# Optimization experiments

Hardware: AMD Instinct MI355X
Metric: run time of the kernel (lower is better)

## Reference

```python
import jax, jax.numpy as jnp
import numpy as np
from jax import lax

B, C, H, W, T = 8, 512, 96, 96, 4
EPS = 1e-5


def setup_inputs() -> dict:
    key = jax.random.key(0)
    k1, k2, k3 = jax.random.split(key, 3)
    x = jax.random.normal(k1, (B, C, H, W), dtype=jnp.float32)
    # grouped 1x1 conv, groups=2: torch weight [C, C//2, 1, 1] -> [2, C//2(out), C//2(in)]
    w_mix = jax.random.normal(k2, (2, C // 2, C // 2), dtype=jnp.float32) * (1.0 / np.sqrt(C // 2))
    # depthwise 3x3: torch weight [C, 1, 3, 3]
    w_dw = jax.random.normal(k3, (C, 1, 3, 3), dtype=jnp.float32) * (1.0 / 3.0)
    gammas = jnp.ones((T, 1, C, 1, 1), dtype=jnp.float32)
    betas = jnp.zeros((T, 1, C, 1, 1), dtype=jnp.float32)
    alpha = jnp.float32(0.25)
    return {"x": x, "w_mix": w_mix, "w_dw": w_dw, "gammas": gammas, "betas": betas, "alpha": alpha}


def _entropy_gate(x):
    gate = jnp.zeros_like(x)
    for d in (1, 2, 4):
        gate = gate + jnp.abs(x - jnp.roll(x, d, axis=2)) + jnp.abs(x - jnp.roll(x, d, axis=3))
    return jax.nn.sigmoid(gate / 3.0)


def reference(x, w_mix, w_dw, gammas, betas, alpha):
    b, c, h_, w_ = x.shape
    x_prev = x
    for t in range(T):
        gate = _entropy_gate(x)
        # grouped 1x1 conv (groups=2): [B,2,C/2,H,W] x [2,Co,Ci] -> [B,2,Co,H,W]
        xg = x.reshape(b, 2, c // 2, h_, w_)
        h = jnp.einsum('bgihw,goi->bgohw', xg, w_mix)
        # channel shuffle: view(B,2,C/2,H,W).transpose(1,2).reshape(B,C,H,W)
        h = h.transpose(0, 2, 1, 3, 4).reshape(b, c, h_, w_)
        # depthwise 3x3, padding=1
        h = lax.conv_general_dilated(h, w_dw, window_strides=(1, 1), padding=((1, 1), (1, 1)),
                                     feature_group_count=c,
                                     dimension_numbers=('NCHW', 'OIHW', 'NCHW'))
        # instance norm (no affine, eps=1e-5) then per-step affine
        mu = jnp.mean(h, axis=(2, 3), keepdims=True)
        var = jnp.mean(jnp.square(h - mu), axis=(2, 3), keepdims=True)
        h = (h - mu) * lax.rsqrt(var + EPS) * gammas[t] + betas[t]
        h = jax.nn.gelu(h, approximate=False)
        x_new = x + gate * h + alpha * (x - x_prev)
        x_prev = x
        x = x_new
    return x
```

## Files before the change

kernel.cpp:

```cpp
#include <hip/hip_runtime.h>
#include <hip/hip_bf16.h>
#include <cstddef>

#define IMW   96
#define HWSZ  (IMW*IMW)
#define CTOT  512
#define CHG   256
#define NBATCH 8
#define ROWP  104
#define XT_LD 280
#define TO_LD 76

typedef short  bf16x8  __attribute__((ext_vector_type(8)));
typedef float  f32x4   __attribute__((ext_vector_type(4)));
typedef unsigned short ushort8v __attribute__((ext_vector_type(8)));
typedef _Float16 f16x2 __attribute__((ext_vector_type(2)));
typedef __fp16   fp16x2b __attribute__((ext_vector_type(2)));

union U32H2 { unsigned u; f16x2 h; fp16x2b hb; };

__device__ __forceinline__ unsigned pk2(float lo, float hi) {
    union { __hip_bfloat162 h; unsigned u; } v;
    v.h = __float22bfloat162_rn(make_float2(lo, hi));
    return v.u;
}
__device__ __forceinline__ unsigned pkh(float lo, float hi) {
    U32H2 v; v.hb = __builtin_amdgcn_cvt_pkrtz(lo, hi); return v.u;
}
__device__ __forceinline__ f16x2 h2(unsigned u) { U32H2 v; v.u = u; return v.h; }
__device__ __forceinline__ unsigned h2u(f16x2 h) { U32H2 v; v.h = h; return v.u; }
__device__ __forceinline__ float bf2f(ushort u) {
    union { unsigned u; float f; } v; v.u = ((unsigned)u) << 16;
    return v.f;
}

__global__ __launch_bounds__(256) void wconv_kernel(const float* __restrict__ w,
                                                    unsigned* __restrict__ wbf) {
    const int i = blockIdx.x * 256 + threadIdx.x;
    wbf[i] = pk2(w[2 * i], w[2 * i + 1]);
}

template<bool XB>
__global__ __launch_bounds__(256, 3) void mix_mfma(
    const void* __restrict__ xin, const ushort* __restrict__ wbf,
    ushort* __restrict__ h)
{
    const int pt = blockIdx.x * 64;
    const int b  = blockIdx.y >> 1, g = blockIdx.y & 1;
    const size_t xoff = ((size_t)b * CTOT + (size_t)g * CHG) * HWSZ;
    const ushort* wg = wbf + (size_t)g * CHG * CHG;
    ushort* hb = h + (size_t)b * CTOT * HWSZ;

    __shared__ ushort XtBuf[19456];

    const int t  = threadIdx.x;
    const int tq = t & 15;
    const int tk = t >> 4;

    #pragma unroll
    for (int it = 0; it < 8; ++it) {
        const int k = 32 * it + 2 * tk;
        unsigned u0, u1, u2, u3;
        if constexpr (XB) {
            const ushort* xb = (const ushort*)xin + xoff;
            ushort4 a0 = *(const ushort4*)&xb[(size_t)k       * HWSZ + pt + 4 * tq];
            ushort4 a1 = *(const ushort4*)&xb[(size_t)(k + 1) * HWSZ + pt + 4 * tq];
            u0 = (unsigned)a0.x | ((unsigned)a1.x << 16);
            u1 = (unsigned)a0.y | ((unsigned)a1.y << 16);
            u2 = (unsigned)a0.z | ((unsigned)a1.z << 16);
            u3 = (unsigned)a0.w | ((unsigned)a1.w << 16);
        } else {
            const float* xb = (const float*)xin + xoff;
            float4 a0 = *(const float4*)&xb[(size_t)k       * HWSZ + pt + 4 * tq];
            float4 a1 = *(const float4*)&xb[(size_t)(k + 1) * HWSZ + pt + 4 * tq];
            u0 = pk2(a0.x, a1.x);
            u1 = pk2(a0.y, a1.y);
            u2 = pk2(a0.z, a1.z);
            u3 = pk2(a0.w, a1.w);
        }
        *(unsigned*)&XtBuf[(4 * tq + 0) * XT_LD + k] = u0;
        *(unsigned*)&XtBuf[(4 * tq + 1) * XT_LD + k] = u1;
        *(unsigned*)&XtBuf[(4 * tq + 2) * XT_LD + k] = u2;
        *(unsigned*)&XtBuf[(4 * tq + 3) * XT_LD + k] = u3;
    }
    __syncthreads();

    const int wv  = t >> 6;
    const int ln  = t & 63;
    const int row = ln & 15;
    const int kb  = ln >> 4;

    f32x4 acc[4][4];
    #pragma unroll
    for (int m = 0; m < 4; ++m)
        #pragma unroll
        for (int n = 0; n < 4; ++n)
            acc[m][n] = (f32x4){0.f, 0.f, 0.f, 0.f};

    #pragma unroll
    for (int ks = 0; ks < 8; ++ks) {
        bf16x8 Xf[4], Wf[4];
        #pragma unroll
        for (int m = 0; m < 4; ++m)
            Xf[m] = *(const bf16x8*)&XtBuf[(16 * m + row) * XT_LD + 32 * ks + 8 * kb];
        #pragma unroll
        for (int n = 0; n < 4; ++n)
            Wf[n] = *(const bf16x8*)&wg[(size_t)(64 * wv + 16 * n + row) * CHG + 32 * ks + 8 * kb];
        #pragma unroll
        for (int m = 0; m < 4; ++m)
            #pragma unroll
            for (int n = 0; n < 4; ++n)
                acc[m][n] = __builtin_amdgcn_mfma_f32_16x16x32_bf16(Xf[m], Wf[n], acc[m][n], 0, 0, 0);
    }

    __syncthreads();
    #pragma unroll
    for (int m = 0; m < 4; ++m) {
        #pragma unroll
        for (int n = 0; n < 4; ++n) {
            const int o = 64 * wv + 16 * n + row;
            *(uint2*)&XtBuf[o * TO_LD + 16 * m + 4 * kb] =
                make_uint2(pkh(acc[m][n][0], acc[m][n][1]), pkh(acc[m][n][2], acc[m][n][3]));
        }
    }
    __syncthreads();
    const int o8i = t >> 3;
    const int px8 = (t & 7) * 8;
    #pragma unroll
    for (int j = 0; j < 8; ++j) {
        const int o2 = o8i + 32 * j;
        const int c  = 2 * o2 + g;
        uint4 v = *(const uint4*)&XtBuf[o2 * TO_LD + px8];
        *(uint4*)&hb[(size_t)c * HWSZ + pt + px8] = v;
    }
}

template<bool XB, bool PB, bool EQ, bool OB>
__global__ __launch_bounds__(576, 4) void plane_kernel(
    const ushort* __restrict__ hmid,
    const void* __restrict__ xcur, const void* __restrict__ xprev,
    const float* __restrict__ wdw,
    const float* __restrict__ gammas, const float* __restrict__ betas,
    const float* __restrict__ alphap, int t,
    void* __restrict__ out)
{
    const int plane = blockIdx.x;
    const int c = plane & (CTOT - 1);
    const ushort* hp = hmid + (size_t)plane * HWSZ;

    __shared__ ushort sh[IMW * ROWP];
    __shared__ ushort sx[IMW * ROWP];
    __shared__ float  red[32];

    const int tid = threadIdx.x;
    const int r   = tid / 6;
    const int s6  = tid - r * 6;
    const int x0  = s6 * 16;
    const int pix = r * IMW + x0;

    ushort8v xr[2];
    float4   xf[4];
    float xv[16];
    if constexpr (XB) {
        const ushort8v* s = (const ushort8v*)((const ushort*)xcur + (size_t)plane * HWSZ + pix);
        xr[0] = s[0]; xr[1] = s[1];
        #pragma unroll
        for (int j = 0; j < 8; ++j) { xv[j] = bf2f(xr[0][j]); xv[8 + j] = bf2f(xr[1][j]); }
    } else {
        const float4* s = (const float4*)((const float*)xcur + (size_t)plane * HWSZ + pix);
        #pragma unroll
        for (int q = 0; q < 4; ++q) xf[q] = s[q];
        #pragma unroll
        for (int q = 0; q < 4; ++q)
            #pragma unroll
            for (int j = 0; j < 4; ++j) xv[4 * q + j] = xf[q][j];
    }
    {
        const uint4* src = (const uint4*)(hp + (size_t)r * IMW);
        uint4* dst = (uint4*)(sh + r * ROWP);
        dst[2 * s6]     = src[2 * s6];
        dst[2 * s6 + 1] = src[2 * s6 + 1];
    }
    {
        uint4* dst = (uint4*)(sx + r * ROWP + x0);
        dst[0] = make_uint4(pkh(xv[0], xv[1]),  pkh(xv[2], xv[3]),
                            pkh(xv[4], xv[5]),  pkh(xv[6], xv[7]));
        dst[1] = make_uint4(pkh(xv[8], xv[9]),  pkh(xv[10], xv[11]),
                            pkh(xv[12], xv[13]), pkh(xv[14], xv[15]));
    }
    float w9[9];
    #pragma unroll
    for (int i = 0; i < 9; ++i) w9[i] = wdw[c * 9 + i];

    __syncthreads();

    ushort8v pr[2];
    float4   pf[4];
    if constexpr (!EQ) {
        if constexpr (PB) {
            const ushort8v* s = (const ushort8v*)((const ushort*)xprev + (size_t)plane * HWSZ + pix);
            pr[0] = s[0]; pr[1] = s[1];
        } else {
            const float4* s = (const float4*)((const float*)xprev + (size_t)plane * HWSZ + pix);
            #pragma unroll
            for (int q = 0; q < 4; ++q) pf[q] = s[q];
        }
    }

    f16x2 cp[8];
    #pragma unroll
    for (int m = 0; m < 8; ++m) cp[m] = (f16x2){(_Float16)0.f, (_Float16)0.f};
    #pragma unroll
    for (int ky = 0; ky < 3; ++ky) {
        const int yy = r + ky - 1;
        if ((unsigned)yy < IMW) {
            const ushort* rp = sh + yy * ROWP + x0;
            uint4 ga = *(const uint4*)rp;
            uint4 gb = *(const uint4*)(rp + 8);
            unsigned gg[8] = {ga.x, ga.y, ga.z, ga.w, gb.x, gb.y, gb.z, gb.w};
            const unsigned L = (s6 > 0) ? *(const unsigned*)(rp - 2)  : 0u;
            const unsigned R = (s6 < 5) ? *(const unsigned*)(rp + 16) : 0u;
            unsigned S[9];
            S[0] = (L >> 16) | (gg[0] << 16);
            #pragma unroll
            for (int m = 1; m < 8; ++m) S[m] = (gg[m - 1] >> 16) | (gg[m] << 16);
            S[8] = (gg[7] >> 16) | (R << 16);
            const _Float16 w0 = (_Float16)w9[3 * ky], w1 = (_Float16)w9[3 * ky + 1],
                           w2 = (_Float16)w9[3 * ky + 2];
            const f16x2 w0_2 = (f16x2){w0, w0}, w1_2 = (f16x2){w1, w1}, w2_2 = (f16x2){w2, w2};
            #pragma unroll
            for (int m = 0; m < 8; ++m)
                cp[m] = cp[m] + w0_2 * h2(S[m]) + w1_2 * h2(gg[m]) + w2_2 * h2(S[m + 1]);
        }
    }
    float conv[16];
    #pragma unroll
    for (int m = 0; m < 8; ++m) { conv[2 * m] = (float)cp[m][0]; conv[2 * m + 1] = (float)cp[m][1]; }

    f16x2 gt2[8];
    #pragma unroll
    for (int m = 0; m < 8; ++m) gt2[m] = (f16x2){(_Float16)0.f, (_Float16)0.f};
    {
        const ushort* xrp = sx + r * ROWP + x0;
        uint4 xa = *(const uint4*)xrp;
        uint4 xb2 = *(const uint4*)(xrp + 8);
        unsigned xc[8] = {xa.x, xa.y, xa.z, xa.w, xb2.x, xb2.y, xb2.z, xb2.w};
        const int lx1 = (x0 == 0) ? (IMW - 2) : (x0 - 2);
        const int lx2 = (x0 == 0) ? (IMW - 4) : (x0 - 4);
        const unsigned L1 = *(const unsigned*)(sx + r * ROWP + lx1);
        const unsigned L2 = *(const unsigned*)(sx + r * ROWP + lx2);
        unsigned p1[8], p2[8], p4[8];
        p1[0] = (L1 >> 16) | (xc[0] << 16);
        #pragma unroll
        for (int m = 1; m < 8; ++m) p1[m] = (xc[m - 1] >> 16) | (xc[m] << 16);
        p2[0] = L1;
        #pragma unroll
        for (int m = 1; m < 8; ++m) p2[m] = xc[m - 1];
        p4[0] = L2; p4[1] = L1;
        #pragma unroll
        for (int m = 2; m < 8; ++m) p4[m] = xc[m - 2];
        #pragma unroll
        for (int m = 0; m < 8; ++m) {
            const f16x2 xcm = h2(xc[m]);
            gt2[m] = gt2[m] + h2(h2u(xcm - h2(p1[m])) & 0x7FFF7FFFu);
            gt2[m] = gt2[m] + h2(h2u(xcm - h2(p2[m])) & 0x7FFF7FFFu);
            gt2[m] = gt2[m] + h2(h2u(xcm - h2(p4[m])) & 0x7FFF7FFFu);
        }
        #pragma unroll
        for (int dd = 0; dd < 3; ++dd) {
            int ym = r - (1 << dd); if (ym < 0) ym += IMW;
            const ushort* vp = sx + ym * ROWP + x0;
            uint4 va = *(const uint4*)vp;
            uint4 vb = *(const uint4*)(vp + 8);
            unsigned vv[8] = {va.x, va.y, va.z, va.w, vb.x, vb.y, vb.z, vb.w};
            #pragma unroll
            for (int m = 0; m < 8; ++m)
                gt2[m] = gt2[m] + h2(h2u(h2(xc[m]) - h2(vv[m])) & 0x7FFF7FFFu);
        }
    }
    float gt[16];
    #pragma unroll
    for (int m = 0; m < 8; ++m) { gt[2 * m] = (float)gt2[m][0]; gt[2 * m + 1] = (float)gt2[m][1]; }

    float s = 0.f, s2 = 0.f;
    #pragma unroll
    for (int i = 0; i < 16; ++i) { s += conv[i]; s2 = fmaf(conv[i], conv[i], s2); }
    #pragma unroll
    for (int off = 32; off; off >>= 1) {
        s  += __shfl_down(s, off, 64);
        s2 += __shfl_down(s2, off, 64);
    }
    const int wv = tid >> 6;
    if ((tid & 63) == 0) { red[wv] = s; red[16 + wv] = s2; }
    __syncthreads();
    float ssum = 0.f, s2sum = 0.f;
    #pragma unroll
    for (int i = 0; i < 9; ++i) { ssum += red[i]; s2sum += red[16 + i]; }
    const float mu   = ssum * (1.f / HWSZ);
    const float var  = fmaxf(s2sum * (1.f / HWSZ) - mu * mu, 0.f);
    const float rsig = rsqrtf(var + 1e-5f);
    const float ga = gammas[t * CTOT + c] * rsig;
    const float be = betas[t * CTOT + c];
    const float alpha = alphap[0];

    #pragma unroll
    for (int half = 0; half < 2; ++half) {
        float pvh[8];
        if constexpr (EQ) {
            #pragma unroll
            for (int j = 0; j < 8; ++j) pvh[j] = xv[8 * half + j];
        } else if constexpr (PB) {
            #pragma unroll
            for (int j = 0; j < 8; ++j) pvh[j] = bf2f(pr[half][j]);
        } else {
            #pragma unroll
            for (int j = 0; j < 4; ++j) { pvh[j] = pf[2 * half][j]; pvh[4 + j] = pf[2 * half + 1][j]; }
        }
        float o8[8];
        #pragma unroll
        for (int i = 0; i < 8; ++i) {
            const int ii = 8 * half + i;
            const float xvi = xv[ii];
            const float hn  = fmaf(conv[ii] - mu, ga, be);
            const float z2  = 1.5957691216f * fmaf(0.044715f * hn * hn, hn, hn);
            const float ea  = __expf(gt[ii] * (-1.f / 3.f));
            const float eb  = __expf(-z2);
            const float den = (1.f + ea) * (1.f + eb);
            const float gg  = hn * __builtin_amdgcn_rcpf(den);
            o8[i] = fmaf(alpha, xvi - pvh[i], xvi + gg);
        }
        if constexpr (OB) {
            uint4 u = make_uint4(pk2(o8[0], o8[1]), pk2(o8[2], o8[3]),
                                 pk2(o8[4], o8[5]), pk2(o8[6], o8[7]));
            *(uint4*)((ushort*)out + (size_t)plane * HWSZ + pix + 8 * half) = u;
        } else {
            float* op = (float*)out + (size_t)plane * HWSZ + pix + 8 * half;
            *(float4*)op       = make_float4(o8[0], o8[1], o8[2], o8[3]);
            *(float4*)(op + 4) = make_float4(o8[4], o8[5], o8[6], o8[7]);
        }
    }
}

extern "C" void kernel_launch(void* const* d_in, const int* in_sizes, int n_in,
                              void* d_out, int out_size, void* d_ws, size_t ws_size,
                              hipStream_t stream) {
    const float* x0     = (const float*)d_in[0];
    const float* wmix   = (const float*)d_in[1];
    const float* wdw    = (const float*)d_in[2];
    const float* gammas = (const float*)d_in[3];
    const float* betas  = (const float*)d_in[4];
    const float* alphap = (const float*)d_in[5];

    const size_t NELEM = (size_t)NBATCH * CTOT * HWSZ;
    float*  D   = (float*)d_out;
    char*   ws  = (char*)d_ws;
    ushort* X1b = (ushort*)ws;
    ushort* X2b = (ushort*)(ws + NELEM * 2);
    ushort* Hb  = (ushort*)(ws + NELEM * 4);
    ushort* Wbf = (ushort*)(ws + NELEM * 6);

    wconv_kernel<<<256, 256, 0, stream>>>(wmix, (unsigned*)Wbf);

    dim3 mgrid(HWSZ / 64, NBATCH * 2);
    const int pgrid = NBATCH * CTOT;

    mix_mfma<false><<<mgrid, 256, 0, stream>>>(x0, Wbf, Hb);
    plane_kernel<false, false, true, true><<<pgrid, 576, 0, stream>>>(
        Hb, x0, x0, wdw, gammas, betas, alphap, 0, X1b);
    mix_mfma<true><<<mgrid, 256, 0, stream>>>(X1b, Wbf, Hb);
    plane_kernel<true, false, false, true><<<pgrid, 576, 0, stream>>>(
        Hb, X1b, x0, wdw, gammas, betas, alphap, 1, X2b);
    mix_mfma<true><<<mgrid, 256, 0, stream>>>(X2b, Wbf, Hb);
    plane_kernel<true, true, false, true><<<pgrid, 576, 0, stream>>>(
        Hb, X2b, X1b, wdw, gammas, betas, alphap, 2, X1b);
    mix_mfma<true><<<mgrid, 256, 0, stream>>>(X1b, Wbf, Hb);
    plane_kernel<true, true, false, false><<<pgrid, 576, 0, stream>>>(
        Hb, X1b, X2b, wdw, gammas, betas, alphap, 3, D);
}
```

Baseline: 556.2 us.

## Switch intermediates to fp16, process two planes per block, stash x0 in output buffer

Replaces bf16 storage and MFMA with fp16 (mfma 16x16x32 f16) for weights, activations and intermediate states. The depthwise plane kernel now handles two batch planes per block, prefetching the second plane's h and x while the first is computed, and splits the exp of the gate into an fp16-packed precompute. x0 is converted to fp16 once and stashed in the output buffer so later steps read half-precision x_prev instead of fp32. This cuts memory traffic and hides latency, at the cost of fp16 range/precision risk and more register pressure.

```diff
diff --git a/kernel.cpp b/kernel.cpp
--- a/kernel.cpp
+++ b/kernel.cpp
@@ -11,44 +11,34 @@
 #define XT_LD 280
 #define TO_LD 76
 
-typedef short  bf16x8  __attribute__((ext_vector_type(8)));
-typedef float  f32x4   __attribute__((ext_vector_type(4)));
-typedef unsigned short ushort8v __attribute__((ext_vector_type(8)));
-typedef _Float16 f16x2 __attribute__((ext_vector_type(2)));
+typedef float    f32x4  __attribute__((ext_vector_type(4)));
+typedef _Float16 f16x8  __attribute__((ext_vector_type(8)));
+typedef _Float16 f16x2  __attribute__((ext_vector_type(2)));
 typedef __fp16   fp16x2b __attribute__((ext_vector_type(2)));
 
 union U32H2 { unsigned u; f16x2 h; fp16x2b hb; };
 
-__device__ __forceinline__ unsigned pk2(float lo, float hi) {
-    union { __hip_bfloat162 h; unsigned u; } v;
-    v.h = __float22bfloat162_rn(make_float2(lo, hi));
-    return v.u;
-}
 __device__ __forceinline__ unsigned pkh(float lo, float hi) {
     U32H2 v; v.hb = __builtin_amdgcn_cvt_pkrtz(lo, hi); return v.u;
 }
 __device__ __forceinline__ f16x2 h2(unsigned u) { U32H2 v; v.u = u; return v.h; }
 __device__ __forceinline__ unsigned h2u(f16x2 h) { U32H2 v; v.h = h; return v.u; }
-__device__ __forceinline__ float bf2f(ushort u) {
-    union { unsigned u; float f; } v; v.u = ((unsigned)u) << 16;
-    return v.f;
-}
 
 __global__ __launch_bounds__(256) void wconv_kernel(const float* __restrict__ w,
-                                                    unsigned* __restrict__ wbf) {
+                                                    unsigned* __restrict__ wh) {
     const int i = blockIdx.x * 256 + threadIdx.x;
-    wbf[i] = pk2(w[2 * i], w[2 * i + 1]);
+    wh[i] = pkh(w[2 * i], w[2 * i + 1]);
 }
 
 template<bool XB>
 __global__ __launch_bounds__(256, 3) void mix_mfma(
-    const void* __restrict__ xin, const ushort* __restrict__ wbf,
+    const void* __restrict__ xin, const ushort* __restrict__ wh,
     ushort* __restrict__ h)
 {
     const int pt = blockIdx.x * 64;
     const int b  = blockIdx.y >> 1, g = blockIdx.y & 1;
     const size_t xoff = ((size_t)b * CTOT + (size_t)g * CHG) * HWSZ;
-    const ushort* wg = wbf + (size_t)g * CHG * CHG;
+    const ushort* wg = wh + (size_t)g * CHG * CHG;
     ushort* hb = h + (size_t)b * CTOT * HWSZ;
 
     __shared__ ushort XtBuf[19456];
@@ -73,10 +63,10 @@
             const float* xb = (const float*)xin + xoff;
             float4 a0 = *(const float4*)&xb[(size_t)k       * HWSZ + pt + 4 * tq];
             float4 a1 = *(const float4*)&xb[(size_t)(k + 1) * HWSZ + pt + 4 * tq];
-            u0 = pk2(a0.x, a1.x);
-            u1 = pk2(a0.y, a1.y);
-            u2 = pk2(a0.z, a1.z);
-            u3 = pk2(a0.w, a1.w);
+            u0 = pkh(a0.x, a1.x);
+            u1 = pkh(a0.y, a1.y);
+            u2 = pkh(a0.z, a1.z);
+            u3 = pkh(a0.w, a1.w);
         }
         *(unsigned*)&XtBuf[(4 * tq + 0) * XT_LD + k] = u0;
         *(unsigned*)&XtBuf[(4 * tq + 1) * XT_LD + k] = u1;
@@ -99,18 +89,18 @@
 
     #pragma unroll
     for (int ks = 0; ks < 8; ++ks) {
-        bf16x8 Xf[4], Wf[4];
+        f16x8 Xf[4], Wf[4];
         #pragma unroll
         for (int m = 0; m < 4; ++m)
-            Xf[m] = *(const bf16x8*)&XtBuf[(16 * m + row) * XT_LD + 32 * ks + 8 * kb];
+            Xf[m] = *(const f16x8*)&XtBuf[(16 * m + row) * XT_LD + 32 * ks + 8 * kb];
         #pragma unroll
         for (int n = 0; n < 4; ++n)
-            Wf[n] = *(const bf16x8*)&wg[(size_t)(64 * wv + 16 * n + row) * CHG + 32 * ks + 8 * kb];
+            Wf[n] = *(const f16x8*)&wg[(size_t)(64 * wv + 16 * n + row) * CHG + 32 * ks + 8 * kb];
         #pragma unroll
         for (int m = 0; m < 4; ++m)
             #pragma unroll
             for (int n = 0; n < 4; ++n)
-                acc[m][n] = __builtin_amdgcn_mfma_f32_16x16x32_bf16(Xf[m], Wf[n], acc[m][n], 0, 0, 0);
+                acc[m][n] = __builtin_amdgcn_mfma_f32_16x16x32_f16(Xf[m], Wf[n], acc[m][n], 0, 0, 0);
     }
 
     __syncthreads();
@@ -135,79 +125,11 @@
     }
 }
 
-template<bool XB, bool PB, bool EQ, bool OB>
-__global__ __launch_bounds__(576, 4) void plane_kernel(
-    const ushort* __restrict__ hmid,
-    const void* __restrict__ xcur, const void* __restrict__ xprev,
-    const float* __restrict__ wdw,
-    const float* __restrict__ gammas, const float* __restrict__ betas,
-    const float* __restrict__ alphap, int t,
-    void* __restrict__ out)
+__device__ __forceinline__ void plane_partA(
+    const ushort* __restrict__ sh, const ushort* __restrict__ sx,
+    float* __restrict__ red, int tid, int r, int s6, int x0,
+    const float* __restrict__ wc, f16x2 (&cp)[8], unsigned (&ea)[8])
 {
-    const int plane = blockIdx.x;
-    const int c = plane & (CTOT - 1);
-    const ushort* hp = hmid + (size_t)plane * HWSZ;
-
-    __shared__ ushort sh[IMW * ROWP];
-    __shared__ ushort sx[IMW * ROWP];
-    __shared__ float  red[32];
-
-    const int tid = threadIdx.x;
-    const int r   = tid / 6;
-    const int s6  = tid - r * 6;
-    const int x0  = s6 * 16;
-    const int pix = r * IMW + x0;
-
-    ushort8v xr[2];
-    float4   xf[4];
-    float xv[16];
-    if constexpr (XB) {
-        const ushort8v* s = (const ushort8v*)((const ushort*)xcur + (size_t)plane * HWSZ + pix);
-        xr[0] = s[0]; xr[1] = s[1];
-        #pragma unroll
-        for (int j = 0; j < 8; ++j) { xv[j] = bf2f(xr[0][j]); xv[8 + j] = bf2f(xr[1][j]); }
-    } else {
-        const float4* s = (const float4*)((const float*)xcur + (size_t)plane * HWSZ + pix);
-        #pragma unroll
-        for (int q = 0; q < 4; ++q) xf[q] = s[q];
-        #pragma unroll
-        for (int q = 0; q < 4; ++q)
-            #pragma unroll
-            for (int j = 0; j < 4; ++j) xv[4 * q + j] = xf[q][j];
-    }
-    {
-        const uint4* src = (const uint4*)(hp + (size_t)r * IMW);
-        uint4* dst = (uint4*)(sh + r * ROWP);
-        dst[2 * s6]     = src[2 * s6];
-        dst[2 * s6 + 1] = src[2 * s6 + 1];
-    }
-    {
-        uint4* dst = (uint4*)(sx + r * ROWP + x0);
-        dst[0] = make_uint4(pkh(xv[0], xv[1]),  pkh(xv[2], xv[3]),
-                            pkh(xv[4], xv[5]),  pkh(xv[6], xv[7]));
-        dst[1] = make_uint4(pkh(xv[8], xv[9]),  pkh(xv[10], xv[11]),
-                            pkh(xv[12], xv[13]), pkh(xv[14], xv[15]));
-    }
-    float w9[9];
-    #pragma unroll
-    for (int i = 0; i < 9; ++i) w9[i] = wdw[c * 9 + i];
-
-    __syncthreads();
-
-    ushort8v pr[2];
-    float4   pf[4];
-    if constexpr (!EQ) {
-        if constexpr (PB) {
-            const ushort8v* s = (const ushort8v*)((const ushort*)xprev + (size_t)plane * HWSZ + pix);
-            pr[0] = s[0]; pr[1] = s[1];
-        } else {
-            const float4* s = (const float4*)((const float*)xprev + (size_t)plane * HWSZ + pix);
-            #pragma unroll
-            for (int q = 0; q < 4; ++q) pf[q] = s[q];
-        }
-    }
-
-    f16x2 cp[8];
     #pragma unroll
     for (int m = 0; m < 8; ++m) cp[m] = (f16x2){(_Float16)0.f, (_Float16)0.f};
     #pragma unroll
@@ -215,9 +137,9 @@
         const int yy = r + ky - 1;
         if ((unsigned)yy < IMW) {
             const ushort* rp = sh + yy * ROWP + x0;
-            uint4 ga = *(const uint4*)rp;
-            uint4 gb = *(const uint4*)(rp + 8);
-            unsigned gg[8] = {ga.x, ga.y, ga.z, ga.w, gb.x, gb.y, gb.z, gb.w};
+            uint4 ga4 = *(const uint4*)rp;
+            uint4 gb4 = *(const uint4*)(rp + 8);
+            unsigned gg[8] = {ga4.x, ga4.y, ga4.z, ga4.w, gb4.x, gb4.y, gb4.z, gb4.w};
             const unsigned L = (s6 > 0) ? *(const unsigned*)(rp - 2)  : 0u;
             const unsigned R = (s6 < 5) ? *(const unsigned*)(rp + 16) : 0u;
             unsigned S[9];
@@ -225,26 +147,22 @@
             #pragma unroll
             for (int m = 1; m < 8; ++m) S[m] = (gg[m - 1] >> 16) | (gg[m] << 16);
             S[8] = (gg[7] >> 16) | (R << 16);
-            const _Float16 w0 = (_Float16)w9[3 * ky], w1 = (_Float16)w9[3 * ky + 1],
-                           w2 = (_Float16)w9[3 * ky + 2];
+            const _Float16 w0 = (_Float16)wc[3 * ky], w1 = (_Float16)wc[3 * ky + 1],
+                           w2 = (_Float16)wc[3 * ky + 2];
             const f16x2 w0_2 = (f16x2){w0, w0}, w1_2 = (f16x2){w1, w1}, w2_2 = (f16x2){w2, w2};
             #pragma unroll
             for (int m = 0; m < 8; ++m)
                 cp[m] = cp[m] + w0_2 * h2(S[m]) + w1_2 * h2(gg[m]) + w2_2 * h2(S[m + 1]);
         }
     }
-    float conv[16];
-    #pragma unroll
-    for (int m = 0; m < 8; ++m) { conv[2 * m] = (float)cp[m][0]; conv[2 * m + 1] = (float)cp[m][1]; }
-
     f16x2 gt2[8];
     #pragma unroll
     for (int m = 0; m < 8; ++m) gt2[m] = (f16x2){(_Float16)0.f, (_Float16)0.f};
     {
         const ushort* xrp = sx + r * ROWP + x0;
-        uint4 xa = *(const uint4*)xrp;
-        uint4 xb2 = *(const uint4*)(xrp + 8);
-        unsigned xc[8] = {xa.x, xa.y, xa.z, xa.w, xb2.x, xb2.y, xb2.z, xb2.w};
+        uint4 xa4 = *(const uint4*)xrp;
+        uint4 xb4 = *(const uint4*)(xrp + 8);
+        unsigned xc[8] = {xa4.x, xa4.y, xa4.z, xa4.w, xb4.x, xb4.y, xb4.z, xb4.w};
         const int lx1 = (x0 == 0) ? (IMW - 2) : (x0 - 2);
         const int lx2 = (x0 == 0) ? (IMW - 4) : (x0 - 4);
         const unsigned L1 = *(const unsigned*)(sx + r * ROWP + lx1);
@@ -278,67 +196,194 @@
                 gt2[m] = gt2[m] + h2(h2u(h2(xc[m]) - h2(vv[m])) & 0x7FFF7FFFu);
         }
     }
-    float gt[16];
-    #pragma unroll
-    for (int m = 0; m < 8; ++m) { gt[2 * m] = (float)gt2[m][0]; gt[2 * m + 1] = (float)gt2[m][1]; }
-
+    #pragma unroll
+    for (int m = 0; m < 8; ++m)
+        ea[m] = pkh(__expf((float)gt2[m][0] * (-1.f / 3.f)),
+                    __expf((float)gt2[m][1] * (-1.f / 3.f)));
     float s = 0.f, s2 = 0.f;
     #pragma unroll
-    for (int i = 0; i < 16; ++i) { s += conv[i]; s2 = fmaf(conv[i], conv[i], s2); }
+    for (int m = 0; m < 8; ++m) {
+        const float c0 = (float)cp[m][0], c1 = (float)cp[m][1];
+        s += c0 + c1;
+        s2 = fmaf(c0, c0, fmaf(c1, c1, s2));
+    }
     #pragma unroll
     for (int off = 32; off; off >>= 1) {
         s  += __shfl_down(s, off, 64);
         s2 += __shfl_down(s2, off, 64);
     }
-    const int wv = tid >> 6;
-    if ((tid & 63) == 0) { red[wv] = s; red[16 + wv] = s2; }
-    __syncthreads();
-    float ssum = 0.f, s2sum = 0.f;
-    #pragma unroll
-    for (int i = 0; i < 9; ++i) { ssum += red[i]; s2sum += red[16 + i]; }
-    const float mu   = ssum * (1.f / HWSZ);
-    const float var  = fmaxf(s2sum * (1.f / HWSZ) - mu * mu, 0.f);
-    const float rsig = rsqrtf(var + 1e-5f);
-    const float ga = gammas[t * CTOT + c] * rsig;
-    const float be = betas[t * CTOT + c];
+    if ((tid & 63) == 0) { red[tid >> 6] = s; red[16 + (tid >> 6)] = s2; }
+}
+
+template<bool EQv, bool OF32v, bool WRXv>
+__device__ __forceinline__ void plane_tail(
+    const ushort* __restrict__ sx, int r, int x0,
+    const f16x2 (&cp)[8], const unsigned (&ea)[8],
+    uint4 pva, uint4 pvb,
+    float mu, float ga, float be, float alpha,
+    size_t gidx, void* __restrict__ out, ushort* __restrict__ xaux)
+{
+    const ushort* xrp = sx + r * ROWP + x0;
+    const uint4 xqa = *(const uint4*)xrp;
+    const uint4 xqb = *(const uint4*)(xrp + 8);
+    const unsigned xu[8] = {xqa.x, xqa.y, xqa.z, xqa.w, xqb.x, xqb.y, xqb.z, xqb.w};
+    unsigned pu[8];
+    if constexpr (!EQv) {
+        pu[0] = pva.x; pu[1] = pva.y; pu[2] = pva.z; pu[3] = pva.w;
+        pu[4] = pvb.x; pu[5] = pvb.y; pu[6] = pvb.z; pu[7] = pvb.w;
+    }
+    float o[16];
+    #pragma unroll
+    for (int m = 0; m < 8; ++m) {
+        const f16x2 xh = h2(xu[m]);
+        const float xv0 = (float)xh[0], xv1 = (float)xh[1];
+        const float c0 = (float)cp[m][0], c1 = (float)cp[m][1];
+        const f16x2 eh = h2(ea[m]);
+        const float e0 = (float)eh[0], e1 = (float)eh[1];
+        const float hn0 = fmaf(c0 - mu, ga, be);
+        const float hn1 = fmaf(c1 - mu, ga, be);
+        const float z20 = 1.5957691216f * fmaf(0.044715f * hn0 * hn0, hn0, hn0);
+        const float z21 = 1.5957691216f * fmaf(0.044715f * hn1 * hn1, hn1, hn1);
+        const float eb0 = __expf(-z20), eb1 = __expf(-z21);
+        const float gg0 = hn0 * __builtin_amdgcn_rcpf((1.f + e0) * (1.f + eb0));
+        const float gg1 = hn1 * __builtin_amdgcn_rcpf((1.f + e1) * (1.f + eb1));
+        float pv0, pv1;
+        if constexpr (EQv) { pv0 = xv0; pv1 = xv1; }
+        else { const f16x2 ph = h2(pu[m]); pv0 = (float)ph[0]; pv1 = (float)ph[1]; }
+        o[2 * m]     = fmaf(alpha, xv0 - pv0, xv0 + gg0);
+        o[2 * m + 1] = fmaf(alpha, xv1 - pv1, xv1 + gg1);
+    }
+    if constexpr (OF32v) {
+        float* op = (float*)out + gidx;
+        *(float4*)(op)      = make_float4(o[0],  o[1],  o[2],  o[3]);
+        *(float4*)(op + 4)  = make_float4(o[4],  o[5],  o[6],  o[7]);
+        *(float4*)(op + 8)  = make_float4(o[8],  o[9],  o[10], o[11]);
+        *(float4*)(op + 12) = make_float4(o[12], o[13], o[14], o[15]);
+    } else {
+        ushort* op = (ushort*)out + gidx;
+        *(uint4*)op       = make_uint4(pkh(o[0], o[1]),   pkh(o[2], o[3]),
+                                       pkh(o[4], o[5]),   pkh(o[6], o[7]));
+        *(uint4*)(op + 8) = make_uint4(pkh(o[8], o[9]),   pkh(o[10], o[11]),
+                                       pkh(o[12], o[13]), pkh(o[14], o[15]));
+    }
+    if constexpr (WRXv) {
+        ushort* xp = xaux + gidx;
+        *(uint4*)xp = xqa; *(uint4*)(xp + 8) = xqb;
+    }
+}
+
+template<bool XF32, bool EQ, bool OF32, bool WRX>
+__global__ __launch_bounds__(576, 4) void plane2_kernel(
+    const ushort* __restrict__ hmid,
+    const void* __restrict__ xcur, const ushort* __restrict__ xprev,
+    const float* __restrict__ wdw,
+    const float* __restrict__ gammas, const float* __restrict__ betas,
+    const float* __restrict__ alphap, int t,
+    void* __restrict__ out, ushort* __restrict__ xaux)
+{
+    __shared__ ushort sh[IMW * ROWP];
+    __shared__ ushort sx[IMW * ROWP];
+    __shared__ float  red[32];
+
+    const int tid = threadIdx.x;
+    const int r   = tid / 6;
+    const int s6  = tid - r * 6;
+    const int x0  = s6 * 16;
+    const int pix = r * IMW + x0;
+    const int c   = blockIdx.x & (CTOT - 1);
+    const int bp  = blockIdx.x >> 9;
+    const size_t off0 = ((size_t)(2 * bp) * CTOT + c) * HWSZ;
+    const size_t off1 = off0 + (size_t)CTOT * HWSZ;
+
+    const float gam   = gammas[t * CTOT + c];
+    const float be    = betas[t * CTOT + c];
     const float alpha = alphap[0];
-
-    #pragma unroll
-    for (int half = 0; half < 2; ++half) {
-        float pvh[8];
-        if constexpr (EQ) {
+    const float* wc   = wdw + c * 9;
+
+    {
+        uint4 xa0, xb0;
+        if constexpr (XF32) {
+            const float4* s = (const float4*)((const float*)xcur + off0 + pix);
+            float4 v0 = s[0], v1 = s[1], v2 = s[2], v3 = s[3];
+            xa0 = make_uint4(pkh(v0.x, v0.y), pkh(v0.z, v0.w), pkh(v1.x, v1.y), pkh(v1.z, v1.w));
+            xb0 = make_uint4(pkh(v2.x, v2.y), pkh(v2.z, v2.w), pkh(v3.x, v3.y), pkh(v3.z, v3.w));
+        } else {
+            const uint4* s = (const uint4*)((const ushort*)xcur + off0 + pix);
+            xa0 = s[0]; xb0 = s[1];
+        }
+        const uint4* hs = (const uint4*)(hmid + off0 + (size_t)r * IMW);
+        uint4 h00 = hs[2 * s6], h01 = hs[2 * s6 + 1];
+        uint4* hd = (uint4*)(sh + r * ROWP);
+        hd[2 * s6] = h00; hd[2 * s6 + 1] = h01;
+        uint4* xd = (uint4*)(sx + r * ROWP + x0);
+        xd[0] = xa0; xd[1] = xb0;
+    }
+    uint4 h10, h11, xa1, xb1;
+    float4 xf1[4];
+    {
+        const uint4* hs = (const uint4*)(hmid + off1 + (size_t)r * IMW);
+        h10 = hs[2 * s6]; h11 = hs[2 * s6 + 1];
+        if constexpr (XF32) {
+            const float4* s = (const float4*)((const float*)xcur + off1 + pix);
             #pragma unroll
-            for (int j = 0; j < 8; ++j) pvh[j] = xv[8 * half + j];
-        } else if constexpr (PB) {
-            #pragma unroll
-            for (int j = 0; j < 8; ++j) pvh[j] = bf2f(pr[half][j]);
+            for (int q = 0; q < 4; ++q) xf1[q] = s[q];
         } else {
-            #pragma unroll
-            for (int j = 0; j < 4; ++j) { pvh[j] = pf[2 * half][j]; pvh[4 + j] = pf[2 * half + 1][j]; }
-        }
-        float o8[8];
-        #pragma unroll
-        for (int i = 0; i < 8; ++i) {
-            const int ii = 8 * half + i;
-            const float xvi = xv[ii];
-            const float hn  = fmaf(conv[ii] - mu, ga, be);
-            const float z2  = 1.5957691216f * fmaf(0.044715f * hn * hn, hn, hn);
-            const float ea  = __expf(gt[ii] * (-1.f / 3.f));
-            const float eb  = __expf(-z2);
-            const float den = (1.f + ea) * (1.f + eb);
-            const float gg  = hn * __builtin_amdgcn_rcpf(den);
-            o8[i] = fmaf(alpha, xvi - pvh[i], xvi + gg);
-        }
-        if constexpr (OB) {
-            uint4 u = make_uint4(pk2(o8[0], o8[1]), pk2(o8[2], o8[3]),
-                                 pk2(o8[4], o8[5]), pk2(o8[6], o8[7]));
-            *(uint4*)((ushort*)out + (size_t)plane * HWSZ + pix + 8 * half) = u;
-        } else {
-            float* op = (float*)out + (size_t)plane * HWSZ + pix + 8 * half;
-            *(float4*)op       = make_float4(o8[0], o8[1], o8[2], o8[3]);
-            *(float4*)(op + 4) = make_float4(o8[4], o8[5], o8[6], o8[7]);
-        }
-    }
+            const uint4* s = (const uint4*)((const ushort*)xcur + off1 + pix);
+            xa1 = s[0]; xb1 = s[1];
+        }
+    }
+    __syncthreads();
+
+    uint4 pa0, pb0;
+    if constexpr (!EQ) {
+        const uint4* s = (const uint4*)(xprev + off0 + pix);
+        pa0 = s[0]; pb0 = s[1];
+    }
+    f16x2 cp[8]; unsigned ea[8];
+    plane_partA(sh, sx, red, tid, r, s6, x0, wc, cp, ea);
+    __syncthreads();
+    float mu, ga;
+    {
+        float ssum = 0.f, s2sum = 0.f;
+        #pragma unroll
+        for (int q = 0; q < 9; ++q) { ssum += red[q]; s2sum += red[16 + q]; }
+        mu = ssum * (1.f / HWSZ);
+        const float var = fmaxf(s2sum * (1.f / HWSZ) - mu * mu, 0.f);
+        ga = gam * rsqrtf(var + 1e-5f);
+    }
+    plane_tail<EQ, OF32, WRX>(sx, r, x0, cp, ea, pa0, pb0, mu, ga, be, alpha,
+                              off0 + pix, out, xaux);
+    if constexpr (XF32) {
+        xa1 = make_uint4(pkh(xf1[0].x, xf1[0].y), pkh(xf1[0].z, xf1[0].w),
+                         pkh(xf1[1].x, xf1[1].y), pkh(xf1[1].z, xf1[1].w));
+        xb1 = make_uint4(pkh(xf1[2].x, xf1[2].y), pkh(xf1[2].z, xf1[2].w),
+                         pkh(xf1[3].x, xf1[3].y), pkh(xf1[3].z, xf1[3].w));
+    }
+    {
+        uint4* hd = (uint4*)(sh + r * ROWP);
+        hd[2 * s6] = h10; hd[2 * s6 + 1] = h11;
+        uint4* xd = (uint4*)(sx + r * ROWP + x0);
+        xd[0] = xa1; xd[1] = xb1;
+    }
+    __syncthreads();
+
+    uint4 pa1, pb1;
+    if constexpr (!EQ) {
+        const uint4* s = (const uint4*)(xprev + off1 + pix);
+        pa1 = s[0]; pb1 = s[1];
+    }
+    plane_partA(sh, sx, red, tid, r, s6, x0, wc, cp, ea);
+    __syncthreads();
+    {
+        float ssum = 0.f, s2sum = 0.f;
+        #pragma unroll
+        for (int q = 0; q < 9; ++q) { ssum += red[q]; s2sum += red[16 + q]; }
+        mu = ssum * (1.f / HWSZ);
+        const float var = fmaxf(s2sum * (1.f / HWSZ) - mu * mu, 0.f);
+        ga = gam * rsqrtf(var + 1e-5f);
+    }
+    plane_tail<EQ, OF32, WRX>(sx, r, x0, cp, ea, pa1, pb1, mu, ga, be, alpha,
+                              off1 + pix, out, xaux);
 }
 
 extern "C" void kernel_launch(void* const* d_in, const int* in_sizes, int n_in,
@@ -353,27 +398,28 @@
 
     const size_t NELEM = (size_t)NBATCH * CTOT * HWSZ;
     float*  D   = (float*)d_out;
+    ushort* X0h = (ushort*)d_out;
     char*   ws  = (char*)d_ws;
-    ushort* X1b = (ushort*)ws;
-    ushort* X2b = (ushort*)(ws + NELEM * 2);
+    ushort* X1h = (ushort*)ws;
+    ushort* X2h = (ushort*)(ws + NELEM * 2);
     ushort* Hb  = (ushort*)(ws + NELEM * 4);
-    ushort* Wbf = (ushort*)(ws + NELEM * 6);
-
-    wconv_kernel<<<256, 256, 0, stream>>>(wmix, (unsigned*)Wbf);
+    ushort* Wh  = (ushort*)(ws + NELEM * 6);
+
+    wconv_kernel<<<256, 256, 0, stream>>>(wmix, (unsigned*)Wh);
 
     dim3 mgrid(HWSZ / 64, NBATCH * 2);
-    const int pgrid = NBATCH * CTOT;
-
-    mix_mfma<false><<<mgrid, 256, 0, stream>>>(x0, Wbf, Hb);
-    plane_kernel<false, false, true, true><<<pgrid, 576, 0, stream>>>(
-        Hb, x0, x0, wdw, gammas, betas, alphap, 0, X1b);
-    mix_mfma<true><<<mgrid, 256, 0, stream>>>(X1b, Wbf, Hb);
-    plane_kernel<true, false, false, true><<<pgrid, 576, 0, stream>>>(
-        Hb, X1b, x0, wdw, gammas, betas, alphap, 1, X2b);
-    mix_mfma<true><<<mgrid, 256, 0, stream>>>(X2b, Wbf, Hb);
-    plane_kernel<true, true, false, true><<<pgrid, 576, 0, stream>>>(
-        Hb, X2b, X1b, wdw, gammas, betas, alphap, 2, X1b);
-    mix_mfma<true><<<mgrid, 256, 0, stream>>>(X1b, Wbf, Hb);
-    plane_kernel<true, true, false, false><<<pgrid, 576, 0, stream>>>(
-        Hb, X1b, X2b, wdw, gammas, betas, alphap, 3, D);
-}
+    const int pgrid2 = (NBATCH / 2) * CTOT;
+
+    mix_mfma<false><<<mgrid, 256, 0, stream>>>(x0, Wh, Hb);
+    plane2_kernel<true, true, false, true><<<pgrid2, 576, 0, stream>>>(
+        Hb, x0, nullptr, wdw, gammas, betas, alphap, 0, X1h, X0h);
+    mix_mfma<true><<<mgrid, 256, 0, stream>>>(X1h, Wh, Hb);
+    plane2_kernel<false, false, false, false><<<pgrid2, 576, 0, stream>>>(
+        Hb, X1h, X0h, wdw, gammas, betas, alphap, 1, X2h, nullptr);
+    mix_mfma<true><<<mgrid, 256, 0, stream>>>(X2h, Wh, Hb);
+    plane2_kernel<false, false, false, false><<<pgrid2, 576, 0, stream>>>(
+        Hb, X2h, X1h, wdw, gammas, betas, alphap, 2, X1h, nullptr);
+    mix_mfma<true><<<mgrid, 256, 0, stream>>>(X1h, Wh, Hb);
+    plane2_kernel<false, false, true, false><<<pgrid2, 576, 0, stream>>>(
+        Hb, X1h, X2h, wdw, gammas, betas, alphap, 3, D, nullptr);
+}
```

Result: slower. 628.5 us (+13.0%).
